# Kernel optimization log

Hardware: AMD Instinct MI355X
Metric: run time of the kernel (lower is better)

The kernel has to match this reference:

```python
import jax, jax.numpy as jnp
import numpy as np

B, N, C, S = 4, 200000, 96, 32
EPS = 1e-05


def setup_inputs() -> dict:
    key = jax.random.key(0)
    kx, kw, kb = jax.random.split(key, 3)
    x = jax.random.normal(kx, (B, N, C), dtype=jnp.float32)
    # Build mutually-consistent CSR offsets (non-empty segments) and per-point segment ids.
    rng = np.random.default_rng(0)
    cuts = np.sort(rng.choice(np.arange(1, N), size=S - 1, replace=False))
    offsets = np.concatenate([[0], cuts, [N]]).astype(np.int64)  # [S+1]
    indices = np.repeat(np.arange(S, dtype=np.int64), np.diff(offsets))  # [N]
    weight = 1.0 + 0.1 * jax.random.normal(kw, (C,), dtype=jnp.float32)
    bias = 0.1 * jax.random.normal(kb, (C,), dtype=jnp.float32)
    return {
        "x": x,
        "batch_offsets": jnp.asarray(offsets),
        "batch_indices": jnp.asarray(indices),
        "weight": weight,
        "bias": bias,
    }


def reference(x, batch_offsets, batch_indices, weight, bias):
    # x: [B, N, C]; batch_offsets: [S+1]; batch_indices: [N]
    counts = (batch_offsets[1:] - batch_offsets[:-1]).astype(x.dtype)  # [S]
    n_seg = counts.shape[0]
    # per-point mean over channels -> segment mean over points (segment_csr 'mean')
    mx = jnp.mean(x, axis=-1)  # [B, N]
    seg_mean = jnp.zeros((x.shape[0], n_seg), x.dtype).at[:, batch_indices].add(mx) / counts  # [B, S]
    nx = x - seg_mean[:, batch_indices, None]  # [B, N, C]
    n2 = jnp.mean(nx * nx, axis=-1)  # [B, N]
    seg_var = jnp.zeros((x.shape[0], n_seg), x.dtype).at[:, batch_indices].add(n2) / counts  # [B, S]
    std = jnp.sqrt(seg_var + EPS)  # [B, S]
    return nx / std[:, batch_indices, None] * weight + bias
```

## Files before the change

### kernel.cpp

```cpp
#include <hip/hip_runtime.h>

#define B_      4
#define N_      200000
#define C_      96
#define S_      32
#define EPS_    1e-5f

#define C4      (C_ / 4)
#define NC4     (N_ * C4)
#define THREADS 256
#define ITER    32
#define CHUNK   (THREADS * ITER)

__global__ __launch_bounds__(THREADS) void stats_kernel(
    const float4* __restrict__ x,
    const int*    __restrict__ seg_of_n,
    float*        __restrict__ gsum,
    float*        __restrict__ gsq)
{
    __shared__ float lsum[S_];
    __shared__ float lsq[S_];
    const int t = threadIdx.x;
    if (t < S_) { lsum[t] = 0.f; lsq[t] = 0.f; }
    __syncthreads();

    const int b = blockIdx.y;
    const float4* xb = x + (size_t)b * NC4;
    const int f0 = blockIdx.x * CHUNK + t;

    int   cur = -1;
    float s1 = 0.f, s2 = 0.f;
    for (int i = 0; i < ITER; ++i) {
        const int f = f0 + i * THREADS;
        if (f >= NC4) break;
        const float4 v = xb[f];
        const int n  = (int)((unsigned)f / 24u);
        const int sg = seg_of_n[n];
        if (sg != cur) {
            if (cur >= 0) { atomicAdd(&lsum[cur], s1); atomicAdd(&lsq[cur], s2); }
            cur = sg; s1 = 0.f; s2 = 0.f;
        }
        s1 += v.x + v.y + v.z + v.w;
        s2 += v.x * v.x + v.y * v.y + v.z * v.z + v.w * v.w;
    }
    if (cur >= 0) { atomicAdd(&lsum[cur], s1); atomicAdd(&lsq[cur], s2); }
    __syncthreads();

    if (t < S_) {
        const float a = lsum[t];
        const float q = lsq[t];
        if (a != 0.f || q != 0.f) {
            atomicAdd(&gsum[b * S_ + t], a);
            atomicAdd(&gsq [b * S_ + t], q);
        }
    }
}

__global__ void finalize_kernel(
    const float* __restrict__ gsum,
    const float* __restrict__ gsq,
    const int*   __restrict__ offsets,
    float*       __restrict__ mean,
    float*       __restrict__ rstd)
{
    const int i = threadIdx.x;
    if (i < B_ * S_) {
        const int s = i % S_;
        const float cnt = (float)(offsets[s + 1] - offsets[s]) * (float)C_;
        const float m = gsum[i] / cnt;
        const float v = gsq[i] / cnt - m * m;
        mean[i] = m;
        rstd[i] = rsqrtf(fmaxf(v, 0.f) + EPS_);
    }
}

__global__ __launch_bounds__(THREADS) void norm_kernel(
    const float4* __restrict__ x,
    const int*    __restrict__ seg_of_n,
    const float4* __restrict__ wgt,
    const float4* __restrict__ bia,
    const float*  __restrict__ mean,
    const float*  __restrict__ rstd,
    float4*       __restrict__ out)
{
    __shared__ float4 lw[C4];
    __shared__ float4 lb[C4];
    const int t = threadIdx.x;
    if (t < C4) { lw[t] = wgt[t]; lb[t] = bia[t]; }
    __syncthreads();

    const int b = blockIdx.y;
    const float4* xb = x   + (size_t)b * NC4;
    float4*       ob = out + (size_t)b * NC4;
    const int f0 = blockIdx.x * CHUNK + t;

    int   cur = -1;
    float m = 0.f, r = 0.f;
    for (int i = 0; i < ITER; ++i) {
        const int f = f0 + i * THREADS;
        if (f >= NC4) break;
        const float4 v = xb[f];
        const int n  = (int)((unsigned)f / 24u);
        const int c  = f - n * 24;
        const int sg = seg_of_n[n];
        if (sg != cur) {
            cur = sg;
            m = mean[b * S_ + sg];
            r = rstd[b * S_ + sg];
        }
        const float4 w  = lw[c];
        const float4 bb = lb[c];
        float4 o;
        o.x = (v.x - m) * r * w.x + bb.x;
        o.y = (v.y - m) * r * w.y + bb.y;
        o.z = (v.z - m) * r * w.z + bb.z;
        o.w = (v.w - m) * r * w.w + bb.w;
        ob[f] = o;
    }
}

extern "C" void kernel_launch(void* const* d_in, const int* in_sizes, int n_in,
                              void* d_out, int out_size, void* d_ws, size_t ws_size,
                              hipStream_t stream)
{
    const float* x       = (const float*)d_in[0];
    const int*   offsets = (const int*)  d_in[1];
    const int*   indices = (const int*)  d_in[2];
    const float* weight  = (const float*)d_in[3];
    const float* bias    = (const float*)d_in[4];
    float*       out     = (float*)d_out;

    float* gsum = (float*)d_ws;
    float* gsq  = gsum + B_ * S_;
    float* mean = gsq  + B_ * S_;
    float* rstd = mean + B_ * S_;

    hipMemsetAsync(d_ws, 0, 2 * B_ * S_ * sizeof(float), stream);

    dim3 grid((NC4 + CHUNK - 1) / CHUNK, B_);
    stats_kernel<<<grid, THREADS, 0, stream>>>(
        (const float4*)x, indices, gsum, gsq);

    finalize_kernel<<<1, 128, 0, stream>>>(gsum, gsq, offsets, mean, rstd);

    norm_kernel<<<grid, THREADS, 0, stream>>>(
        (const float4*)x, indices, (const float4*)weight, (const float4*)bias,
        mean, rstd, (float4*)out);
}
```

Before: 594.4 us.

## Replace per-point segment lookup with CSR offset search and fold normalization into FMA

Both kernels stop reading the per-point segment-index array. Each thread instead binary-searches the CSR offsets cached in shared memory and then walks segments incrementally with strength-reduced index math. ITER becomes 30 so the chunk divides the data exactly, which removes the bounds checks. The norm kernel caches mean/rstd in shared memory and precomputes per-thread scale and shift vectors, since each thread only touches three channel positions. It then runs a single FMA per element, traverses in reverse, and writes output with nontemporal stores. This trades the index-array traffic and the divisions for more complex control flow, and it relies on the exact tiling of N.

```diff
diff --git a/kernel.cpp b/kernel.cpp
--- a/kernel.cpp
+++ b/kernel.cpp
@@ -9,41 +9,65 @@
 #define C4      (C_ / 4)
 #define NC4     (N_ * C4)
 #define THREADS 256
-#define ITER    32
+#define ITER    30
 #define CHUNK   (THREADS * ITER)
+#define GRIDX   (NC4 / CHUNK)
+#define GROUPS  (ITER / 3)
+
+typedef float f32x4 __attribute__((ext_vector_type(4)));
+
+__device__ __forceinline__ float4 scale4(const float4 a, const float s) {
+    return make_float4(a.x * s, a.y * s, a.z * s, a.w * s);
+}
+__device__ __forceinline__ float4 nms4(const float4 bb, const float m, const float4 fw) {
+    return make_float4(bb.x - m * fw.x, bb.y - m * fw.y, bb.z - m * fw.z, bb.w - m * fw.w);
+}
 
 __global__ __launch_bounds__(THREADS) void stats_kernel(
     const float4* __restrict__ x,
-    const int*    __restrict__ seg_of_n,
+    const int*    __restrict__ offsets,
     float*        __restrict__ gsum,
     float*        __restrict__ gsq)
 {
+    __shared__ int   soff[S_ + 1];
     __shared__ float lsum[S_];
-    __shared__ float lsq[S_];
+    __shared__ float lsq [S_];
     const int t = threadIdx.x;
-    if (t < S_) { lsum[t] = 0.f; lsq[t] = 0.f; }
+    if (t <= S_) soff[t] = offsets[t];
+    if (t <  S_) { lsum[t] = 0.f; lsq[t] = 0.f; }
     __syncthreads();
 
     const int b = blockIdx.y;
     const float4* xb = x + (size_t)b * NC4;
     const int f0 = blockIdx.x * CHUNK + t;
 
-    int   cur = -1;
+    int n = f0 / 24;
+    int c = f0 - n * 24;
+    int sg = 0;
+    #pragma unroll
+    for (int st = 16; st; st >>= 1) {
+        const int cand = sg + st;
+        if (soff[cand] <= n) sg = cand;
+    }
+    int nxt = soff[sg + 1];
+
     float s1 = 0.f, s2 = 0.f;
-    for (int i = 0; i < ITER; ++i) {
-        const int f = f0 + i * THREADS;
-        if (f >= NC4) break;
-        const float4 v = xb[f];
-        const int n  = (int)((unsigned)f / 24u);
-        const int sg = seg_of_n[n];
-        if (sg != cur) {
-            if (cur >= 0) { atomicAdd(&lsum[cur], s1); atomicAdd(&lsq[cur], s2); }
-            cur = sg; s1 = 0.f; s2 = 0.f;
+    for (int k = 0; k < ITER; ++k) {
+        if (n >= nxt) {
+            atomicAdd(&lsum[sg], s1);
+            atomicAdd(&lsq [sg], s2);
+            s1 = 0.f; s2 = 0.f;
+            do { ++sg; } while (soff[sg + 1] <= n);
+            nxt = soff[sg + 1];
         }
-        s1 += v.x + v.y + v.z + v.w;
+        const float4 v = xb[f0 + k * THREADS];
+        s1 += (v.x + v.y) + (v.z + v.w);
         s2 += v.x * v.x + v.y * v.y + v.z * v.z + v.w * v.w;
-    }
-    if (cur >= 0) { atomicAdd(&lsum[cur], s1); atomicAdd(&lsq[cur], s2); }
+        c += 16; if (c >= 24) { c -= 24; ++n; }
+        n += 10;
+    }
+    atomicAdd(&lsum[sg], s1);
+    atomicAdd(&lsq [sg], s2);
     __syncthreads();
 
     if (t < S_) {
@@ -76,47 +100,79 @@
 
 __global__ __launch_bounds__(THREADS) void norm_kernel(
     const float4* __restrict__ x,
-    const int*    __restrict__ seg_of_n,
+    const int*    __restrict__ offsets,
     const float4* __restrict__ wgt,
     const float4* __restrict__ bia,
     const float*  __restrict__ mean,
     const float*  __restrict__ rstd,
     float4*       __restrict__ out)
 {
+    __shared__ int    soff[S_ + 1];
     __shared__ float4 lw[C4];
     __shared__ float4 lb[C4];
+    __shared__ float  lm[S_];
+    __shared__ float  lr[S_];
     const int t = threadIdx.x;
-    if (t < C4) { lw[t] = wgt[t]; lb[t] = bia[t]; }
+    const int b = blockIdx.y;
+    if (t <= S_) soff[t] = offsets[t];
+    if (t <  C4) { lw[t] = wgt[t]; lb[t] = bia[t]; }
+    if (t <  S_) { lm[t] = mean[b * S_ + t]; lr[t] = rstd[b * S_ + t]; }
     __syncthreads();
 
-    const int b = blockIdx.y;
     const float4* xb = x   + (size_t)b * NC4;
     float4*       ob = out + (size_t)b * NC4;
     const int f0 = blockIdx.x * CHUNK + t;
 
-    int   cur = -1;
-    float m = 0.f, r = 0.f;
-    for (int i = 0; i < ITER; ++i) {
-        const int f = f0 + i * THREADS;
-        if (f >= NC4) break;
-        const float4 v = xb[f];
-        const int n  = (int)((unsigned)f / 24u);
-        const int c  = f - n * 24;
-        const int sg = seg_of_n[n];
-        if (sg != cur) {
-            cur = sg;
-            m = mean[b * S_ + sg];
-            r = rstd[b * S_ + sg];
-        }
-        const float4 w  = lw[c];
-        const float4 bb = lb[c];
-        float4 o;
-        o.x = (v.x - m) * r * w.x + bb.x;
-        o.y = (v.y - m) * r * w.y + bb.y;
-        o.z = (v.z - m) * r * w.z + bb.z;
-        o.w = (v.w - m) * r * w.w + bb.w;
-        ob[f] = o;
-    }
+    const int c0 = f0 - (f0 / 24) * 24;
+    int c1 = c0 + 16; if (c1 >= 24) c1 -= 24;
+    int c2 = c0 + 8;  if (c2 >= 24) c2 -= 24;
+
+    const int fhi = f0 + (ITER - 1) * THREADS;
+    int n = fhi / 24;
+    int c = fhi - n * 24;
+
+    int sg = 0;
+    #pragma unroll
+    for (int st = 16; st; st >>= 1) {
+        const int cand = sg + st;
+        if (soff[cand] <= n) sg = cand;
+    }
+    int lo = soff[sg];
+
+    float4 fw0, fb0, fw1, fb1, fw2, fb2;
+#define RECOMP() { \
+        const float m_ = lm[sg], r_ = lr[sg]; \
+        fw0 = scale4(lw[c0], r_); fb0 = nms4(lb[c0], m_, fw0); \
+        fw1 = scale4(lw[c1], r_); fb1 = nms4(lb[c1], m_, fw1); \
+        fw2 = scale4(lw[c2], r_); fb2 = nms4(lb[c2], m_, fw2); \
+    }
+    RECOMP();
+
+#define NBODY(K, J) { \
+        if (n < lo) {                                    \
+            do { --sg; } while (n < soff[sg]);           \
+            lo = soff[sg]; \
+            RECOMP(); \
+        } \
+        const int fi = f0 + (K) * THREADS; \
+        const float4 v = xb[fi]; \
+        float4 o; \
+        o.x = v.x * fw##J.x + fb##J.x; \
+        o.y = v.y * fw##J.y + fb##J.y; \
+        o.z = v.z * fw##J.z + fb##J.z; \
+        o.w = v.w * fw##J.w + fb##J.w; \
+        __builtin_nontemporal_store(*(const f32x4*)&o, (f32x4*)(ob + fi)); \
+        c -= 16; if (c < 0) { c += 24; --n; } \
+        n -= 10; \
+    }
+
+    for (int g = GROUPS - 1; g >= 0; --g) {
+        NBODY(3 * g + 2, 2)
+        NBODY(3 * g + 1, 1)
+        NBODY(3 * g + 0, 0)
+    }
+#undef NBODY
+#undef RECOMP
 }
 
 extern "C" void kernel_launch(void* const* d_in, const int* in_sizes, int n_in,
@@ -129,6 +185,7 @@
     const float* weight  = (const float*)d_in[3];
     const float* bias    = (const float*)d_in[4];
     float*       out     = (float*)d_out;
+    (void)indices; (void)in_sizes; (void)n_in; (void)out_size; (void)ws_size;
 
     float* gsum = (float*)d_ws;
     float* gsq  = gsum + B_ * S_;
@@ -137,13 +194,13 @@
 
     hipMemsetAsync(d_ws, 0, 2 * B_ * S_ * sizeof(float), stream);
 
-    dim3 grid((NC4 + CHUNK - 1) / CHUNK, B_);
+    dim3 grid(GRIDX, B_);
     stats_kernel<<<grid, THREADS, 0, stream>>>(
-        (const float4*)x, indices, gsum, gsq);
+        (const float4*)x, offsets, gsum, gsq);
 
     finalize_kernel<<<1, 128, 0, stream>>>(gsum, gsq, offsets, mean, rstd);
 
     norm_kernel<<<grid, THREADS, 0, stream>>>(
-        (const float4*)x, indices, (const float4*)weight, (const float4*)bias,
+        (const float4*)x, offsets, (const float4*)weight, (const float4*)bias,
         mean, rstd, (float4*)out);
 }
```

Measured after the change: 571.5 us. 3.8% less time.
